# Optimization experiments

Measured on AMD Instinct MI355X. Metric: run time of the kernel, lower is better.

## Reference

```python
import jax, jax.numpy as jnp
import numpy as np

IN_FEATURES = 4096
OUT_FEATURES = 11008
W_BITS = 4
GROUP_SIZE = 128
NUM_CHERRIES = 128                       # ceil(4096*0.03125)//8*8
NUM_NORMAL = IN_FEATURES - NUM_CHERRIES  # 3968
N_GROUPS = NUM_NORMAL // GROUP_SIZE      # 31
QROWS = NUM_NORMAL // 8 * W_BITS         # 1984 packed uint8 rows
QMIN = -(2 ** (W_BITS - 1))              # signed int4 min = -8
BATCH = 64


def setup_inputs() -> dict:
    key = jax.random.key(0)
    k1, k2, k3, k4, k5 = jax.random.split(key, 5)
    x = jax.random.normal(k1, (BATCH, IN_FEATURES), jnp.float32)
    # packed 4-bit weights: two nibbles per uint8, stored as [QROWS, out]
    qweight = jax.random.randint(k2, (QROWS, OUT_FEATURES), 0, 256, jnp.int32).astype(jnp.uint8)
    # per-group scales, stored transposed as [n_groups, out]
    scales = jax.random.uniform(k3, (N_GROUPS, OUT_FEATURES), jnp.float32, 0.005, 0.02)
    # full-precision outlier ('cherry') columns, stored as [num_cherries, out]
    cherry_weight = jax.random.normal(k4, (NUM_CHERRIES, OUT_FEATURES), jnp.float32) * 0.02
    rng = np.random.default_rng(0)
    cherry_indices = jnp.asarray(
        np.sort(rng.choice(IN_FEATURES, NUM_CHERRIES, replace=False)).astype(np.int32))
    bias = jax.random.normal(k5, (OUT_FEATURES,), jnp.float32) * 0.01
    return {"x": x, "qweight": qweight, "cherry_weight": cherry_weight,
            "cherry_indices": cherry_indices, "scales": scales, "bias": bias}


def _normal_indices(cherry_indices):
    # complement of cherry_indices, as in the torch scatter/nonzero construction
    mask = jnp.ones((IN_FEATURES,), dtype=bool).at[cherry_indices].set(False)
    return jnp.nonzero(mask, size=NUM_NORMAL)[0]  # static size -> jit ok


def reference(x, qweight, cherry_weight, cherry_indices, scales, bias):
    # --- unpack 4-bit weights (matches QuantLinear.unpack for w_bits=4) ---
    q = qweight.T                                    # [out, QROWS]
    nib = jnp.stack([q & 0xF, (q >> 4) & 0xF], axis=-1)  # low nibble first
    nib = nib.reshape(OUT_FEATURES, NUM_NORMAL)
    intw = nib.astype(jnp.int32) + QMIN              # signed int4 values
    # --- dequantize: repeat-interleave per-group scales along in dim ---
    s = jnp.repeat(scales.T, GROUP_SIZE, axis=1)     # [out, NUM_NORMAL]
    w_normal = intw.astype(s.dtype) * s              # dequantized normal weight
    # --- merge cherry outlier columns via column-gather on x (same math as
    #     scattering into a full [out, in] weight then x @ W.T) ---
    normal_idx = _normal_indices(cherry_indices)
    out = x[:, normal_idx] @ w_normal.T + x[:, cherry_indices] @ cherry_weight
    return out + bias
```

## Files before the change

### kernel.cpp

```cpp
#include <hip/hip_runtime.h>
#include <hip/hip_bf16.h>
#include <stdint.h>

#define IN_F 4096
#define OUT_F 11008
#define NUM_CH 128
#define NUM_NORM 3968
#define BATCH 64
#define KSPLIT 8
#define KCHUNK (IN_F / KSPLIT)
#define NMEGA (KCHUNK / 128)
#define BS 136

typedef short short8 __attribute__((ext_vector_type(8)));
typedef float float4v __attribute__((ext_vector_type(4)));
typedef int int4v __attribute__((ext_vector_type(4)));

__device__ __forceinline__ void barrier_no_vmcnt() {
    asm volatile("s_waitcnt lgkmcnt(0)\n\ts_barrier" ::: "memory");
}

__device__ __forceinline__ unsigned short f2bf(float f) {
    union { float f; unsigned u; } v; v.f = f;
    unsigned u = v.u;
    return (unsigned short)((u + 0x7FFFu + ((u >> 16) & 1u)) >> 16);
}

__device__ __forceinline__ unsigned pk_bf16(float lo, float hi) {
    __hip_bfloat162 h = __float22bfloat162_rn(make_float2(lo, hi));
    union { __hip_bfloat162 h; unsigned u; } c; c.h = h; return c.u;
}

__global__ __launch_bounds__(256) void permute_x(
        const float* __restrict__ x, const int* __restrict__ cidx,
        unsigned short* __restrict__ xp) {
    int i = blockIdx.x * blockDim.x + threadIdx.x;
    int b = blockIdx.y;
    int lo = 0, hi = NUM_CH;
    while (lo < hi) { int mid = (lo + hi) >> 1; if (cidx[mid] < i) lo = mid + 1; else hi = mid; }
    bool isch = (lo < NUM_CH) && (cidx[lo] == i);
    int pos = isch ? (NUM_NORM + lo) : (i - lo);
    xp[b * IN_F + pos] = f2bf(x[b * IN_F + i]);
}

__global__ __launch_bounds__(256) void reduce_out(
        const float* __restrict__ part, const float* __restrict__ bias,
        float* __restrict__ out) {
    const int i = blockIdx.x * 256 + threadIdx.x;
    const int c = i % (OUT_F / 4);
    float4v s = *reinterpret_cast<const float4v*>(bias + c * 4);
    #pragma unroll
    for (int ky = 0; ky < KSPLIT; ++ky) {
        const float4v p = reinterpret_cast<const float4v*>(
            part + (size_t)ky * BATCH * OUT_F)[i];
        s = (float4v){s[0] + p[0], s[1] + p[1], s[2] + p[2], s[3] + p[3]};
    }
    reinterpret_cast<float4v*>(out)[i] = s;
}

__global__ __launch_bounds__(256, 4) void qgemm(
        const unsigned short* __restrict__ xp, const int* __restrict__ qw,
        const float* __restrict__ cw, const float* __restrict__ scales,
        float* __restrict__ part) {
    __shared__ unsigned short Bt[2][64][BS];

    const int tid  = threadIdx.x;
    const int wave = tid >> 6;
    const int lane = tid & 63;
    const int ln   = lane & 15;
    const int lq   = lane >> 4;
    const int n0    = blockIdx.x * 64;
    const int kbase = blockIdx.y * KCHUNK;
    const int tcol = (tid & 15) << 2;
    const int trow = tid >> 4;

    const int*   qbase = qw + n0 + tcol;
    const float* sbase = scales + n0 + tcol;
    const float* cbase = cw + n0 + tcol;

    float4v acc[4];
    #pragma unroll
    for (int s = 0; s < 4; ++s) acc[s] = (float4v){0.f, 0.f, 0.f, 0.f};

    int4v qcur[4]; float4v scur;
    {
        const int rb = (kbase >> 1) + 4 * trow;
        #pragma unroll
        for (int i = 0; i < 4; ++i)
            qcur[i] = *reinterpret_cast<const int4v*>(qbase + (size_t)(rb + i) * OUT_F);
        scur = *reinterpret_cast<const float4v*>(sbase + (size_t)(kbase >> 7) * OUT_F);
    }

    for (int s = 0; s < NMEGA; ++s) {
        const int k0 = kbase + s * 128;
        unsigned short (*buf)[BS] = Bt[s & 1];

        if (k0 < NUM_NORM) {
            const int4v q0 = qcur[0], q1 = qcur[1], q2 = qcur[2], q3 = qcur[3];
            const float4v sc = scur;
            const int kn = k0 + 128;
            if (s + 1 < NMEGA && kn < NUM_NORM) {
                const int rb = (kn >> 1) + 4 * trow;
                #pragma unroll
                for (int i = 0; i < 4; ++i)
                    qcur[i] = *reinterpret_cast<const int4v*>(qbase + (size_t)(rb + i) * OUT_F);
                scur = *reinterpret_cast<const float4v*>(sbase + (size_t)(kn >> 7) * OUT_F);
            }
            const int4v qq[4] = {q0, q1, q2, q3};
            #pragma unroll
            for (int cc = 0; cc < 4; ++cc) {
                union { short8 v; unsigned u[4]; } wv;
                const float s1 = sc[cc];
                #pragma unroll
                for (int i = 0; i < 4; ++i) {
                    const int q = qq[i][cc];
                    wv.u[i] = pk_bf16((float)((q & 0xF) - 8) * s1,
                                      (float)(((q >> 4) & 0xF) - 8) * s1);
                }
                *reinterpret_cast<short8*>(&buf[tcol + cc][trow * 8]) = wv.v;
            }
        } else {
            float4v ch[8];
            #pragma unroll
            for (int j = 0; j < 8; ++j)
                ch[j] = *reinterpret_cast<const float4v*>(
                    cbase + (size_t)(8 * trow + j) * OUT_F);
            #pragma unroll
            for (int cc = 0; cc < 4; ++cc) {
                union { short8 v; unsigned u[4]; } wv;
                #pragma unroll
                for (int m = 0; m < 4; ++m)
                    wv.u[m] = pk_bf16(ch[2 * m][cc], ch[2 * m + 1][cc]);
                *reinterpret_cast<short8*>(&buf[tcol + cc][trow * 8]) = wv.v;
            }
        }

        barrier_no_vmcnt();

        const unsigned short* xprow =
            xp + (size_t)((wave << 4) + ln) * IN_F + k0 + (lq << 3);
        const short8 a0 = *reinterpret_cast<const short8*>(xprow);
        const short8 a1 = *reinterpret_cast<const short8*>(xprow + 32);
        const short8 a2 = *reinterpret_cast<const short8*>(xprow + 64);
        const short8 a3 = *reinterpret_cast<const short8*>(xprow + 96);

        #pragma unroll
        for (int st = 0; st < 4; ++st) {
            const unsigned short* bp = &buf[(st << 4) + ln][lq << 3];
            acc[st] = __builtin_amdgcn_mfma_f32_16x16x32_bf16(
                a0, *reinterpret_cast<const short8*>(bp), acc[st], 0, 0, 0);
            acc[st] = __builtin_amdgcn_mfma_f32_16x16x32_bf16(
                a1, *reinterpret_cast<const short8*>(bp + 32), acc[st], 0, 0, 0);
            acc[st] = __builtin_amdgcn_mfma_f32_16x16x32_bf16(
                a2, *reinterpret_cast<const short8*>(bp + 64), acc[st], 0, 0, 0);
            acc[st] = __builtin_amdgcn_mfma_f32_16x16x32_bf16(
                a3, *reinterpret_cast<const short8*>(bp + 96), acc[st], 0, 0, 0);
        }
    }

    float* pbase = part + (size_t)blockIdx.y * BATCH * OUT_F;
    #pragma unroll
    for (int st = 0; st < 4; ++st) {
        const int n = n0 + (st << 4) + ln;
        #pragma unroll
        for (int r = 0; r < 4; ++r) {
            const int m = (wave << 4) + (lq << 2) + r;
            pbase[(size_t)m * OUT_F + n] = acc[st][r];
        }
    }
}

extern "C" void kernel_launch(void* const* d_in, const int* in_sizes, int n_in,
                              void* d_out, int out_size, void* d_ws, size_t ws_size,
                              hipStream_t stream) {
    const float* x      = (const float*)d_in[0];
    const int*   qw     = (const int*)d_in[1];
    const float* cw     = (const float*)d_in[2];
    const int*   cidx   = (const int*)d_in[3];
    const float* scales = (const float*)d_in[4];
    const float* bias   = (const float*)d_in[5];
    float*       out    = (float*)d_out;

    unsigned short* xp   = (unsigned short*)d_ws;
    float*          part = (float*)((char*)d_ws + (512 << 10));

    dim3 pgrid(IN_F / 256, BATCH);
    permute_x<<<pgrid, 256, 0, stream>>>(x, cidx, xp);
    qgemm<<<dim3(OUT_F / 64, KSPLIT), 256, 0, stream>>>(xp, qw, cw, scales, part);
    reduce_out<<<(BATCH * OUT_F / 4) / 256, 256, 0, stream>>>(part, bias, out);
}
```

Baseline: 161.1 us.

## Double K-split, preload activations in registers, and remap waves to output columns

```diff
diff --git a/kernel.cpp b/kernel.cpp
--- a/kernel.cpp
+++ b/kernel.cpp
@@ -7,9 +7,9 @@
 #define NUM_CH 128
 #define NUM_NORM 3968
 #define BATCH 64
-#define KSPLIT 8
+#define KSPLIT 16
 #define KCHUNK (IN_F / KSPLIT)
-#define NMEGA (KCHUNK / 128)
+#define NMEGA 2
 #define BS 136
 
 typedef short short8 __attribute__((ext_vector_type(8)));
@@ -58,7 +58,7 @@
     reinterpret_cast<float4v*>(out)[i] = s;
 }
 
-__global__ __launch_bounds__(256, 4) void qgemm(
+__global__ __launch_bounds__(256, 2) void qgemm(
         const unsigned short* __restrict__ xp, const int* __restrict__ qw,
         const float* __restrict__ cw, const float* __restrict__ scales,
         float* __restrict__ part) {
@@ -70,7 +70,8 @@
     const int ln   = lane & 15;
     const int lq   = lane >> 4;
     const int n0    = blockIdx.x * 64;
-    const int kbase = blockIdx.y * KCHUNK;
+    const int ky    = blockIdx.y;
+    const int kbase = ky * KCHUNK;
     const int tcol = (tid & 15) << 2;
     const int trow = tid >> 4;
 
@@ -78,33 +79,46 @@
     const float* sbase = scales + n0 + tcol;
     const float* cbase = cw + n0 + tcol;
 
+    short8 a_all[4][8];
+    #pragma unroll
+    for (int mt = 0; mt < 4; ++mt) {
+        const unsigned short* ap = xp + (size_t)(mt * 16 + ln) * IN_F + kbase + (lq << 3);
+        #pragma unroll
+        for (int j = 0; j < 8; ++j)
+            a_all[mt][j] = *reinterpret_cast<const short8*>(ap + j * 32);
+    }
+    int4v qc[4];
+    {
+        const int rb = (kbase >> 1) + 4 * trow;
+        #pragma unroll
+        for (int i = 0; i < 4; ++i)
+            qc[i] = *reinterpret_cast<const int4v*>(qbase + (size_t)(rb + i) * OUT_F);
+    }
+    float4v sc0 = *reinterpret_cast<const float4v*>(
+        sbase + (size_t)(kbase >> 7) * OUT_F);
+    float4v sc1 = sc0;
+    const bool m1_normal = (kbase + 128 < NUM_NORM);
+    if (m1_normal)
+        sc1 = *reinterpret_cast<const float4v*>(
+            sbase + (size_t)((kbase >> 7) + 1) * OUT_F);
+
     float4v acc[4];
     #pragma unroll
     for (int s = 0; s < 4; ++s) acc[s] = (float4v){0.f, 0.f, 0.f, 0.f};
 
-    int4v qcur[4]; float4v scur;
-    {
-        const int rb = (kbase >> 1) + 4 * trow;
-        #pragma unroll
-        for (int i = 0; i < 4; ++i)
-            qcur[i] = *reinterpret_cast<const int4v*>(qbase + (size_t)(rb + i) * OUT_F);
-        scur = *reinterpret_cast<const float4v*>(sbase + (size_t)(kbase >> 7) * OUT_F);
-    }
-
+    #pragma unroll
     for (int s = 0; s < NMEGA; ++s) {
         const int k0 = kbase + s * 128;
-        unsigned short (*buf)[BS] = Bt[s & 1];
+        unsigned short (*buf)[BS] = Bt[s];
 
-        if (k0 < NUM_NORM) {
-            const int4v q0 = qcur[0], q1 = qcur[1], q2 = qcur[2], q3 = qcur[3];
-            const float4v sc = scur;
-            const int kn = k0 + 128;
-            if (s + 1 < NMEGA && kn < NUM_NORM) {
-                const int rb = (kn >> 1) + 4 * trow;
+        if (s == 0 || m1_normal) {
+            const int4v q0 = qc[0], q1 = qc[1], q2 = qc[2], q3 = qc[3];
+            const float4v sc = (s == 0) ? sc0 : sc1;
+            if (s == 0 && m1_normal) {
+                const int rb = ((k0 + 128) >> 1) + 4 * trow;
                 #pragma unroll
                 for (int i = 0; i < 4; ++i)
-                    qcur[i] = *reinterpret_cast<const int4v*>(qbase + (size_t)(rb + i) * OUT_F);
-                scur = *reinterpret_cast<const float4v*>(sbase + (size_t)(kn >> 7) * OUT_F);
+                    qc[i] = *reinterpret_cast<const int4v*>(qbase + (size_t)(rb + i) * OUT_F);
             }
             const int4v qq[4] = {q0, q1, q2, q3};
             #pragma unroll
@@ -137,35 +151,29 @@
 
         barrier_no_vmcnt();
 
-        const unsigned short* xprow =
-            xp + (size_t)((wave << 4) + ln) * IN_F + k0 + (lq << 3);
-        const short8 a0 = *reinterpret_cast<const short8*>(xprow);
-        const short8 a1 = *reinterpret_cast<const short8*>(xprow + 32);
-        const short8 a2 = *reinterpret_cast<const short8*>(xprow + 64);
-        const short8 a3 = *reinterpret_cast<const short8*>(xprow + 96);
+        const unsigned short* brow = &buf[(wave << 4) + ln][lq << 3];
+        const short8 b0 = *reinterpret_cast<const short8*>(brow);
+        const short8 b1 = *reinterpret_cast<const short8*>(brow + 32);
+        const short8 b2 = *reinterpret_cast<const short8*>(brow + 64);
+        const short8 b3 = *reinterpret_cast<const short8*>(brow + 96);
 
         #pragma unroll
-        for (int st = 0; st < 4; ++st) {
-            const unsigned short* bp = &buf[(st << 4) + ln][lq << 3];
-            acc[st] = __builtin_amdgcn_mfma_f32_16x16x32_bf16(
-                a0, *reinterpret_cast<const short8*>(bp), acc[st], 0, 0, 0);
-            acc[st] = __builtin_amdgcn_mfma_f32_16x16x32_bf16(
-                a1, *reinterpret_cast<const short8*>(bp + 32), acc[st], 0, 0, 0);
-            acc[st] = __builtin_amdgcn_mfma_f32_16x16x32_bf16(
-                a2, *reinterpret_cast<const short8*>(bp + 64), acc[st], 0, 0, 0);
-            acc[st] = __builtin_amdgcn_mfma_f32_16x16x32_bf16(
-                a3, *reinterpret_cast<const short8*>(bp + 96), acc[st], 0, 0, 0);
+        for (int mt = 0; mt < 4; ++mt) {
+            acc[mt] = __builtin_amdgcn_mfma_f32_16x16x32_bf16(a_all[mt][s * 4 + 0], b0, acc[mt], 0, 0, 0);
+            acc[mt] = __builtin_amdgcn_mfma_f32_16x16x32_bf16(a_all[mt][s * 4 + 1], b1, acc[mt], 0, 0, 0);
+            acc[mt] = __builtin_amdgcn_mfma_f32_16x16x32_bf16(a_all[mt][s * 4 + 2], b2, acc[mt], 0, 0, 0);
+            acc[mt] = __builtin_amdgcn_mfma_f32_16x16x32_bf16(a_all[mt][s * 4 + 3], b3, acc[mt], 0, 0, 0);
         }
     }
 
     float* pbase = part + (size_t)blockIdx.y * BATCH * OUT_F;
+    const int n = n0 + (wave << 4) + ln;
     #pragma unroll
-    for (int st = 0; st < 4; ++st) {
-        const int n = n0 + (st << 4) + ln;
+    for (int mt = 0; mt < 4; ++mt) {
         #pragma unroll
         for (int r = 0; r < 4; ++r) {
-            const int m = (wave << 4) + (lq << 2) + r;
-            pbase[(size_t)m * OUT_F + n] = acc[st][r];
+            const int m = mt * 16 + (lq << 2) + r;
+            pbase[(size_t)m * OUT_F + n] = acc[mt][r];
         }
     }
 }
```

Measured after the change: 184.6 us. +14.6%, slower.
